# Kernel optimization log

Hardware: AMD Instinct MI355X
Metric: run time of the kernel (lower is better)

Reference implementation:

```python
import jax, jax.numpy as jnp
import numpy as np

B, S, H, E, TOP_K = 4, 4096, 4096, 64, 2

def setup_inputs() -> dict:
    key = jax.random.key(0)
    k1, k2 = jax.random.split(key)
    hidden_states = jax.random.normal(k1, (B, S, H), dtype=jnp.float32)
    gate_weight = jax.random.normal(k2, (E, H), dtype=jnp.float32) * (H ** -0.5)
    return {"hidden_states": hidden_states, "gate_weight": gate_weight}

def reference(hidden_states, gate_weight):
    # gate: logits[b,s,e] = hidden[b,s,h] @ W[e,h]^T (nn.Linear, no bias)
    router_logits = jnp.einsum('bsh,eh->bse', hidden_states, gate_weight)
    router_probs = jax.nn.softmax(router_logits, axis=-1)
    # top-k over experts, then renormalize the selected weights
    expert_weights, expert_indices = jax.lax.top_k(router_probs, TOP_K)
    expert_weights = expert_weights / jnp.sum(expert_weights, axis=-1, keepdims=True)
    return (router_probs, expert_indices, expert_weights)
```

## Files before the change

kernel.cpp:

```cpp
#include <hip/hip_runtime.h>
#include <math.h>

#define TOKENS 16384
#define HDIM 4096
#define NE 64

#define BM 64
#define BK 32
#define NKG 2
#define KSLICE (HDIM / NKG)
#define LDSP 68
#define TILE (BK * LDSP)

__global__ __launch_bounds__(512, 2) void router_fused(const float* __restrict__ A,
                                                       const float* __restrict__ W,
                                                       float* __restrict__ out) {
  __shared__ float smem[NKG * 2 * TILE];

  const int tid = threadIdx.x;
  const int kg = tid >> 8;
  const int t = tid & 255;
  const int bt = blockIdx.x;

  const int sr = t >> 2;
  const int sc = (t & 3) * 4;

  const float* Ab = A + (size_t)(bt * BM + sr) * HDIM + (size_t)kg * KSLICE + sc;
  const float* Wb = W + (size_t)sr * HDIM + (size_t)kg * KSLICE + sc;

  float* As = smem + kg * (2 * TILE);
  float* Ws = As + TILE;

  const int tx = t & 15;
  const int ty = t >> 4;

  float acc[4][4];
#pragma unroll
  for (int i = 0; i < 4; ++i)
#pragma unroll
    for (int j = 0; j < 4; ++j) acc[i][j] = 0.f;

  float4 a0 = *(const float4*)(Ab);
  float4 a1 = *(const float4*)(Ab + 16);
  float4 w0 = *(const float4*)(Wb);
  float4 w1 = *(const float4*)(Wb + 16);

  for (int kc = 0; kc < KSLICE; kc += BK) {
    As[(sc + 0) * LDSP + sr] = a0.x;
    As[(sc + 1) * LDSP + sr] = a0.y;
    As[(sc + 2) * LDSP + sr] = a0.z;
    As[(sc + 3) * LDSP + sr] = a0.w;
    As[(sc + 16) * LDSP + sr] = a1.x;
    As[(sc + 17) * LDSP + sr] = a1.y;
    As[(sc + 18) * LDSP + sr] = a1.z;
    As[(sc + 19) * LDSP + sr] = a1.w;
    Ws[(sc + 0) * LDSP + sr] = w0.x;
    Ws[(sc + 1) * LDSP + sr] = w0.y;
    Ws[(sc + 2) * LDSP + sr] = w0.z;
    Ws[(sc + 3) * LDSP + sr] = w0.w;
    Ws[(sc + 16) * LDSP + sr] = w1.x;
    Ws[(sc + 17) * LDSP + sr] = w1.y;
    Ws[(sc + 18) * LDSP + sr] = w1.z;
    Ws[(sc + 19) * LDSP + sr] = w1.w;
    __syncthreads();

    if (kc + BK < KSLICE) {
      a0 = *(const float4*)(Ab + kc + BK);
      a1 = *(const float4*)(Ab + kc + BK + 16);
      w0 = *(const float4*)(Wb + kc + BK);
      w1 = *(const float4*)(Wb + kc + BK + 16);
    }

#pragma unroll
    for (int k = 0; k < BK; ++k) {
      float4 av = *(const float4*)&As[k * LDSP + ty * 4];
      float4 wv = *(const float4*)&Ws[k * LDSP + tx * 4];
      const float a[4] = {av.x, av.y, av.z, av.w};
      const float w[4] = {wv.x, wv.y, wv.z, wv.w};
#pragma unroll
      for (int i = 0; i < 4; ++i)
#pragma unroll
        for (int j = 0; j < 4; ++j) acc[i][j] = fmaf(a[i], w[j], acc[i][j]);
    }
    __syncthreads();
  }

  float* L = smem;
  if (kg == 0) {
#pragma unroll
    for (int i = 0; i < 4; ++i)
      *(float4*)&L[(ty * 4 + i) * LDSP + tx * 4] =
          make_float4(acc[i][0], acc[i][1], acc[i][2], acc[i][3]);
  }
  __syncthreads();
  if (kg == 1) {
#pragma unroll
    for (int i = 0; i < 4; ++i) {
      float4* p = (float4*)&L[(ty * 4 + i) * LDSP + tx * 4];
      float4 v = *p;
      *p = make_float4(v.x + acc[i][0], v.y + acc[i][1], v.z + acc[i][2],
                       v.w + acc[i][3]);
    }
  }
  __syncthreads();

  const int lane = tid & 63;
  const int wv8 = tid >> 6;
#pragma unroll
  for (int r = 0; r < 8; ++r) {
    const int lt = wv8 * 8 + r;
    const int tok = bt * BM + lt;
    const float l = L[lt * LDSP + lane];

    float m = l;
#pragma unroll
    for (int off = 32; off >= 1; off >>= 1) m = fmaxf(m, __shfl_xor(m, off, 64));

    const float e = expf(l - m);
    float sum = e;
#pragma unroll
    for (int off = 32; off >= 1; off >>= 1) sum += __shfl_xor(sum, off, 64);

    const float p = e / sum;
    out[(size_t)tok * NE + lane] = p;

    float m0 = p;
#pragma unroll
    for (int off = 32; off >= 1; off >>= 1) m0 = fmaxf(m0, __shfl_xor(m0, off, 64));
    const unsigned long long b0 = __ballot(p == m0);
    const int i0 = __ffsll(b0) - 1;

    const float pm = (lane == i0) ? -1.f : p;
    float m1 = pm;
#pragma unroll
    for (int off = 32; off >= 1; off >>= 1) m1 = fmaxf(m1, __shfl_xor(m1, off, 64));
    const unsigned long long b1 = __ballot(pm == m1);
    const int i1 = __ffsll(b1) - 1;

    if (lane == 0) {
      float* idxo = out + (size_t)TOKENS * NE + (size_t)tok * 2;
      idxo[0] = (float)i0;
      idxo[1] = (float)i1;
      float* wo = out + (size_t)TOKENS * NE + (size_t)TOKENS * 2 + (size_t)tok * 2;
      const float d = m0 + m1;
      wo[0] = m0 / d;
      wo[1] = m1 / d;
    }
  }
}

extern "C" void kernel_launch(void* const* d_in, const int* in_sizes, int n_in,
                              void* d_out, int out_size, void* d_ws, size_t ws_size,
                              hipStream_t stream) {
  const float* A = (const float*)d_in[0];
  const float* W = (const float*)d_in[1];
  float* out = (float*)d_out;
  (void)d_ws;

  router_fused<<<dim3(TOKENS / BM), 512, 0, stream>>>(A, W, out);
}
```

Baseline: 395.5 us.

## Replace FP32 FMA GEMM with split-bf16 MFMA using hi/lo decomposition

The scalar FP32 outer-product gate GEMM is replaced with MFMA bf16 16x16x32 instructions. Each operand is split into a high and low bf16 part, and four MFMA products are accumulated to approach FP32 accuracy. A small pre-kernel converts W into hi/lo bf16 arrays in the workspace, and A is split on the fly when staged into XOR-swizzled LDS. The intent is to move the matmul onto the matrix cores. The costs are the extra launch, the conversion arithmetic, and a small accuracy loss compared with true FP32.

```diff
diff --git a/kernel.cpp b/kernel.cpp
--- a/kernel.cpp
+++ b/kernel.cpp
@@ -6,111 +6,139 @@
 #define NE 64
 
 #define BM 64
-#define BK 32
-#define NKG 2
-#define KSLICE (HDIM / NKG)
-#define LDSP 68
-#define TILE (BK * LDSP)
+#define BK 64
+#define LP 68
 
-__global__ __launch_bounds__(512, 2) void router_fused(const float* __restrict__ A,
-                                                       const float* __restrict__ W,
-                                                       float* __restrict__ out) {
-  __shared__ float smem[NKG * 2 * TILE];
+typedef float f32x4 __attribute__((ext_vector_type(4)));
+typedef int i32x4 __attribute__((ext_vector_type(4)));
+typedef __bf16 bf16x8 __attribute__((ext_vector_type(8)));
+
+__device__ __forceinline__ void split8(f32x4 v0, f32x4 v1, i32x4& h, i32x4& l) {
+  float x[8];
+#pragma unroll
+  for (int j = 0; j < 4; ++j) { x[j] = v0[j]; x[4 + j] = v1[j]; }
+  union { unsigned short u[8]; i32x4 v; } H, L;
+#pragma unroll
+  for (int j = 0; j < 8; ++j) {
+    __bf16 hb = (__bf16)x[j];
+    H.u[j] = __builtin_bit_cast(unsigned short, hb);
+    L.u[j] = __builtin_bit_cast(unsigned short, (__bf16)(x[j] - (float)hb));
+  }
+  h = H.v; l = L.v;
+}
+
+__device__ __forceinline__ f32x4 mfma_bf16(i32x4 a, i32x4 b, f32x4 c) {
+  return __builtin_amdgcn_mfma_f32_16x16x32_bf16(
+      __builtin_bit_cast(bf16x8, a), __builtin_bit_cast(bf16x8, b), c, 0, 0, 0);
+}
+
+__global__ __launch_bounds__(256) void convert_w(const float* __restrict__ W,
+                                                 unsigned short* __restrict__ Wh,
+                                                 unsigned short* __restrict__ Wl) {
+  const int i = (blockIdx.x * 256 + threadIdx.x) * 8;
+  f32x4 v0 = *(const f32x4*)(W + i);
+  f32x4 v1 = *(const f32x4*)(W + i + 4);
+  i32x4 h, l;
+  split8(v0, v1, h, l);
+  *(i32x4*)(Wh + i) = h;
+  *(i32x4*)(Wl + i) = l;
+}
+
+__global__ __launch_bounds__(512, 2) void router_mfma(const float* __restrict__ A,
+                                                      const unsigned short* __restrict__ Wh,
+                                                      const unsigned short* __restrict__ Wl,
+                                                      float* __restrict__ out) {
+  __shared__ __align__(16) unsigned short smem[4 * BM * BK];
+  unsigned short* AhS = smem;
+  unsigned short* AlS = smem + BM * BK;
+  unsigned short* WhS = smem + 2 * BM * BK;
+  unsigned short* WlS = smem + 3 * BM * BK;
 
   const int tid = threadIdx.x;
-  const int kg = tid >> 8;
-  const int t = tid & 255;
   const int bt = blockIdx.x;
 
-  const int sr = t >> 2;
-  const int sc = (t & 3) * 4;
+  const int srow = tid >> 3;
+  const int sc = tid & 7;
+  const int soff = srow * BK + ((sc ^ (srow & 7)) << 3);
 
-  const float* Ab = A + (size_t)(bt * BM + sr) * HDIM + (size_t)kg * KSLICE + sc;
-  const float* Wb = W + (size_t)sr * HDIM + (size_t)kg * KSLICE + sc;
+  const float* Ab = A + (size_t)(bt * BM + srow) * HDIM + sc * 8;
+  const unsigned short* Whb = Wh + srow * HDIM + sc * 8;
+  const unsigned short* Wlb = Wl + srow * HDIM + sc * 8;
 
-  float* As = smem + kg * (2 * TILE);
-  float* Ws = As + TILE;
+  const int lane = tid & 63;
+  const int wv = tid >> 6;
+  const int tg = wv & 3;
+  const int eg = wv >> 2;
+  const int l15 = lane & 15;
+  const int l7 = lane & 7;
+  const int fko = lane >> 4;
+  const int arow = tg * 16 + l15;
+  const int brow = eg * 32 + l15;
 
-  const int tx = t & 15;
-  const int ty = t >> 4;
+  f32x4 acc0 = {0.f, 0.f, 0.f, 0.f};
+  f32x4 acc1 = {0.f, 0.f, 0.f, 0.f};
 
-  float acc[4][4];
-#pragma unroll
-  for (int i = 0; i < 4; ++i)
-#pragma unroll
-    for (int j = 0; j < 4; ++j) acc[i][j] = 0.f;
+  f32x4 a0 = *(const f32x4*)(Ab);
+  f32x4 a1 = *(const f32x4*)(Ab + 4);
+  i32x4 whr = *(const i32x4*)(Whb);
+  i32x4 wlr = *(const i32x4*)(Wlb);
 
-  float4 a0 = *(const float4*)(Ab);
-  float4 a1 = *(const float4*)(Ab + 16);
-  float4 w0 = *(const float4*)(Wb);
-  float4 w1 = *(const float4*)(Wb + 16);
-
-  for (int kc = 0; kc < KSLICE; kc += BK) {
-    As[(sc + 0) * LDSP + sr] = a0.x;
-    As[(sc + 1) * LDSP + sr] = a0.y;
-    As[(sc + 2) * LDSP + sr] = a0.z;
-    As[(sc + 3) * LDSP + sr] = a0.w;
-    As[(sc + 16) * LDSP + sr] = a1.x;
-    As[(sc + 17) * LDSP + sr] = a1.y;
-    As[(sc + 18) * LDSP + sr] = a1.z;
-    As[(sc + 19) * LDSP + sr] = a1.w;
-    Ws[(sc + 0) * LDSP + sr] = w0.x;
-    Ws[(sc + 1) * LDSP + sr] = w0.y;
-    Ws[(sc + 2) * LDSP + sr] = w0.z;
-    Ws[(sc + 3) * LDSP + sr] = w0.w;
-    Ws[(sc + 16) * LDSP + sr] = w1.x;
-    Ws[(sc + 17) * LDSP + sr] = w1.y;
-    Ws[(sc + 18) * LDSP + sr] = w1.z;
-    Ws[(sc + 19) * LDSP + sr] = w1.w;
+  for (int kc = BK;; kc += BK) {
+    i32x4 ah, al;
+    split8(a0, a1, ah, al);
+    *(i32x4*)&AhS[soff] = ah;
+    *(i32x4*)&AlS[soff] = al;
+    *(i32x4*)&WhS[soff] = whr;
+    *(i32x4*)&WlS[soff] = wlr;
     __syncthreads();
 
-    if (kc + BK < KSLICE) {
-      a0 = *(const float4*)(Ab + kc + BK);
-      a1 = *(const float4*)(Ab + kc + BK + 16);
-      w0 = *(const float4*)(Wb + kc + BK);
-      w1 = *(const float4*)(Wb + kc + BK + 16);
+    if (kc < HDIM) {
+      a0 = *(const f32x4*)(Ab + kc);
+      a1 = *(const f32x4*)(Ab + kc + 4);
+      whr = *(const i32x4*)(Whb + kc);
+      wlr = *(const i32x4*)(Wlb + kc);
     }
 
 #pragma unroll
-    for (int k = 0; k < BK; ++k) {
-      float4 av = *(const float4*)&As[k * LDSP + ty * 4];
-      float4 wv = *(const float4*)&Ws[k * LDSP + tx * 4];
-      const float a[4] = {av.x, av.y, av.z, av.w};
-      const float w[4] = {wv.x, wv.y, wv.z, wv.w};
-#pragma unroll
-      for (int i = 0; i < 4; ++i)
-#pragma unroll
-        for (int j = 0; j < 4; ++j) acc[i][j] = fmaf(a[i], w[j], acc[i][j]);
+    for (int ks = 0; ks < 2; ++ks) {
+      const int ch = ks * 4 + fko;
+      const int aoff = arow * BK + ((ch ^ l7) << 3);
+      const int boff = brow * BK + ((ch ^ l7) << 3);
+      i32x4 fah = *(const i32x4*)&AhS[aoff];
+      i32x4 fal = *(const i32x4*)&AlS[aoff];
+      i32x4 fbh0 = *(const i32x4*)&WhS[boff];
+      i32x4 fbl0 = *(const i32x4*)&WlS[boff];
+      i32x4 fbh1 = *(const i32x4*)&WhS[boff + 16 * BK];
+      i32x4 fbl1 = *(const i32x4*)&WlS[boff + 16 * BK];
+      acc0 = mfma_bf16(fah, fbh0, acc0);
+      acc1 = mfma_bf16(fah, fbh1, acc1);
+      acc0 = mfma_bf16(fal, fbh0, acc0);
+      acc1 = mfma_bf16(fal, fbh1, acc1);
+      acc0 = mfma_bf16(fah, fbl0, acc0);
+      acc1 = mfma_bf16(fah, fbl1, acc1);
+      acc0 = mfma_bf16(fal, fbl0, acc0);
+      acc1 = mfma_bf16(fal, fbl1, acc1);
     }
+    if (kc >= HDIM) break;
     __syncthreads();
   }
 
-  float* L = smem;
-  if (kg == 0) {
+  __syncthreads();
+  float* L = (float*)smem;
 #pragma unroll
-    for (int i = 0; i < 4; ++i)
-      *(float4*)&L[(ty * 4 + i) * LDSP + tx * 4] =
-          make_float4(acc[i][0], acc[i][1], acc[i][2], acc[i][3]);
-  }
-  __syncthreads();
-  if (kg == 1) {
-#pragma unroll
-    for (int i = 0; i < 4; ++i) {
-      float4* p = (float4*)&L[(ty * 4 + i) * LDSP + tx * 4];
-      float4 v = *p;
-      *p = make_float4(v.x + acc[i][0], v.y + acc[i][1], v.z + acc[i][2],
-                       v.w + acc[i][3]);
-    }
+  for (int r = 0; r < 4; ++r) {
+    const int row = tg * 16 + fko * 4 + r;
+    L[row * LP + eg * 32 + l15] = acc0[r];
+    L[row * LP + eg * 32 + 16 + l15] = acc1[r];
   }
   __syncthreads();
 
-  const int lane = tid & 63;
   const int wv8 = tid >> 6;
 #pragma unroll
   for (int r = 0; r < 8; ++r) {
     const int lt = wv8 * 8 + r;
     const int tok = bt * BM + lt;
-    const float l = L[lt * LDSP + lane];
+    const float l = L[lt * LP + lane];
 
     float m = l;
 #pragma unroll
@@ -155,7 +183,9 @@
   const float* A = (const float*)d_in[0];
   const float* W = (const float*)d_in[1];
   float* out = (float*)d_out;
-  (void)d_ws;
+  unsigned short* Whi = (unsigned short*)d_ws;
+  unsigned short* Wlo = Whi + (size_t)NE * HDIM;
 
-  router_fused<<<dim3(TOKENS / BM), 512, 0, stream>>>(A, W, out);
+  convert_w<<<dim3(NE * HDIM / (256 * 8)), 256, 0, stream>>>(W, Whi, Wlo);
+  router_mfma<<<dim3(TOKENS / BM), 512, 0, stream>>>(A, Whi, Wlo, out);
 }
```

Result: no change. 395.6 us (+0.0%).
